# Kernel tuning notes

Measured on AMD Instinct MI355X. Metric: run time of the kernel, lower is better.

## Reference

```python
import jax, jax.numpy as jnp
import numpy as np

A_NUM = 9
C_NUM = 20

def setup_inputs() -> dict:
    key = jax.random.key(0)
    ks = jax.random.split(key, 12)
    B, Cin, H, W = 32, 256, 56, 56
    hidden = 256
    N, M = 64, 2048
    out_ch = 5 * A_NUM + C_NUM
    features = jax.random.normal(ks[0], (B, Cin, H, W), jnp.float32)
    w1 = jax.random.normal(ks[1], (hidden, Cin), jnp.float32) * (1.0 / np.sqrt(Cin))
    b1 = jax.random.normal(ks[2], (hidden,), jnp.float32) * 0.01
    w2 = jax.random.normal(ks[3], (out_ch, hidden), jnp.float32) * (1.0 / np.sqrt(hidden))
    b2 = jax.random.normal(ks[4], (out_ch,), jnp.float32) * 0.01
    # anchor shapes (w, h), positive sizes in grid units
    anc = 1.0 + 5.0 * jax.random.uniform(ks[5], (A_NUM, 2), jnp.float32)
    # grid of cell centers
    xs = jnp.arange(W, dtype=jnp.float32) + 0.5
    ys = jnp.arange(H, dtype=jnp.float32) + 0.5
    gx, gy = jnp.meshgrid(xs, ys, indexing='xy')  # (H, W)
    grid = jnp.broadcast_to(jnp.stack([gx, gy], axis=-1)[None], (B, H, W, 2))
    # GT boxes (x1, y1, x2, y2, cls) with x1<x2, y1<y2
    x1 = jax.random.uniform(ks[6], (B, N), jnp.float32) * (W - 9.0)
    y1 = jax.random.uniform(ks[7], (B, N), jnp.float32) * (H - 9.0)
    bw = 1.0 + 7.0 * jax.random.uniform(ks[8], (B, N), jnp.float32)
    bh = 1.0 + 7.0 * jax.random.uniform(ks[9], (B, N), jnp.float32)
    cls = jax.random.randint(ks[10], (B, N), 0, C_NUM).astype(jnp.float32)
    bboxes = jnp.stack([x1, y1, x1 + bw, y1 + bh, cls], axis=-1)
    total_anchors = B * A_NUM * H * W
    pos_anchor_idx = jax.random.randint(ks[11], (M,), 0, total_anchors, jnp.int64 if jax.config.jax_enable_x64 else jnp.int32)
    neg_anchor_idx = jax.random.randint(jax.random.fold_in(key, 99), (M,), 0, total_anchors, jnp.int64 if jax.config.jax_enable_x64 else jnp.int32)
    GT_offsets = jax.random.normal(jax.random.fold_in(key, 100), (M, 4), jnp.float32) * 0.1
    return {"features": features, "w1": w1, "b1": b1, "w2": w2, "b2": b2,
            "anc": anc, "grid": grid, "bboxes": bboxes, "GT_offsets": GT_offsets,
            "pos_anchor_idx": pos_anchor_idx, "neg_anchor_idx": neg_anchor_idx}

def _generate_anchor(anc, grid):
    # grid: (B,H,W,2), anc: (A,2) -> anchors (B,A,H,W,4) as (x1,y1,x2,y2)
    g = grid[:, None]                      # (B,1,H,W,2)
    a = anc[None, :, None, None]           # (1,A,1,1,2)
    return jnp.concatenate([g - a / 2, g + a / 2], axis=-1)

def _generate_proposal_yolo(anchors, offsets):
    ctr = (anchors[..., :2] + anchors[..., 2:]) / 2
    wh = anchors[..., 2:] - anchors[..., :2]
    new_wh = wh * jnp.exp(offsets[..., 2:])
    new_ctr = ctr + offsets[..., :2]
    return jnp.concatenate([new_ctr - new_wh / 2, new_ctr + new_wh / 2], axis=-1)

def _iou(proposals, bboxes):
    # proposals (B,A,H,W,4) -> (B,AHW,4); bboxes (B,N,5) -> iou (B,AHW,N)
    B = proposals.shape[0]
    p = proposals.reshape(B, -1, 4)[:, :, None, :]   # (B,AHW,1,4)
    g = bboxes[:, None, :, :]                        # (B,1,N,5)
    ix1 = jnp.maximum(p[..., 0], g[..., 0])
    iy1 = jnp.maximum(p[..., 1], g[..., 1])
    ix2 = jnp.minimum(p[..., 2], g[..., 2])
    iy2 = jnp.minimum(p[..., 3], g[..., 3])
    inter = jnp.clip(ix2 - ix1, 0) * jnp.clip(iy2 - iy1, 0)
    gt_area = (bboxes[:, :, 2] - bboxes[:, :, 0]) * (bboxes[:, :, 3] - bboxes[:, :, 1])
    p_area = (p[..., 2] - p[..., 0]) * (p[..., 3] - p[..., 1])
    return inter / (gt_area[:, None, :] + p_area - inter)

def reference(features, w1, b1, w2, b2, anc, grid, bboxes, GT_offsets,
              pos_anchor_idx, neg_anchor_idx):
    B, _, H, W = features.shape
    A = anc.shape[0]
    M = pos_anchor_idx.shape[0]
    # PredictionNetwork (dropout in eval = identity), 1x1 convs as einsum
    x = jnp.einsum('bchw,oc->bohw', features, w1) + b1[None, :, None, None]
    x = jax.nn.leaky_relu(x, 0.01)
    x = jnp.einsum('bchw,oc->bohw', x, w2) + b2[None, :, None, None]
    anc_data = x[:, :5 * A].reshape(B, A, 5, H, W)
    class_all = x[:, 5 * A:]                               # (B,C,H,W)
    conf_all = jax.nn.sigmoid(anc_data[:, :, 0])           # (B,A,H,W)
    offsets_all = jnp.transpose(anc_data[:, :, 1:5], (0, 1, 3, 4, 2))  # (B,A,H,W,4)
    # training extraction
    conf_flat = conf_all.reshape(-1)
    conf_scores = jnp.concatenate([conf_flat[pos_anchor_idx], conf_flat[neg_anchor_idx]])[:, None]  # (2M,1)
    offsets_pos = offsets_all.reshape(-1, 4)[pos_anchor_idx]            # (M,4)
    # class scores for positive anchors: index arithmetic over (B,A,H,W)
    bi = pos_anchor_idx // (A * H * W)
    hw = pos_anchor_idx % (H * W)
    hi, wi = hw // W, hw % W
    class_pos = class_all[bi, :, hi, wi]                                # (M,C)
    # anchors -> proposals -> IoU
    anchors = _generate_anchor(anc, grid)
    proposals = _generate_proposal_yolo(anchors, offsets_all)
    iou_mat = _iou(proposals, bboxes)                                   # (B,AHW,N)
    # YOLO SSE losses
    gt_conf = jnp.concatenate([jnp.ones((M, 1), conf_scores.dtype), jnp.zeros((M, 1), conf_scores.dtype)])
    conf_loss = jnp.sum((conf_scores - gt_conf) ** 2) / (2 * M)
    reg_loss = jnp.sum((offsets_pos - GT_offsets) ** 2) / M
    total_loss = conf_loss + reg_loss
    return total_loss, iou_mat, class_pos
```

## Files before the change

kernel.cpp:

```cpp
#include <hip/hip_runtime.h>
#include <math.h>

#define B_    32
#define CIN   256
#define HID   256
#define OC    65
#define A_    9
#define H_    56
#define W_    56
#define HW    3136
#define AHW   28224
#define NBOX  64
#define M_    2048
#define CNUM  20
#define NTILE 49

#define IOU_N ((size_t)B_ * AHW * NBOX)
#define X2_BYTES ((size_t)B_ * OC * HW * 4)

#define FOFF(frag) (((frag) << 3) + ((((frag) >> 3)) << 3))

typedef _Float16 half8 __attribute__((ext_vector_type(8)));
typedef float f32x16 __attribute__((ext_vector_type(16)));
typedef float f32x4  __attribute__((ext_vector_type(4)));

__device__ __forceinline__ unsigned int pkh(float a, float b) {
    _Float16 ha = (_Float16)a, hb = (_Float16)b;
    unsigned short ua = __builtin_bit_cast(unsigned short, ha);
    unsigned short ub = __builtin_bit_cast(unsigned short, hb);
    return (unsigned int)ua | ((unsigned int)ub << 16);
}

__global__ __launch_bounds__(256) void prep_kernel(
    const float* __restrict__ w1, const float* __restrict__ w2,
    _Float16* __restrict__ w1s, _Float16* __restrict__ w2s)
{
    const int f = blockIdx.x * 256 + threadIdx.x;
    {
        const int e    = f & 7;
        const int lane = (f >> 3) & 63;
        const int kc   = (f >> 9) & 15;
        const int ob   = f >> 13;
        const int row  = ob * 32 + (lane & 31);
        const int k    = kc * 16 + (lane >> 5) * 8 + e;
        w1s[f] = (_Float16)w1[row * CIN + k];
    }
    if (f < 20480) {
        const int e    = f & 7;
        const int lane = (f >> 3) & 63;
        const int ks2  = (f >> 9) & 7;
        const int rt   = f >> 12;
        const int row  = rt * 16 + (lane & 15);
        const int k    = ks2 * 32 + (lane >> 4) * 8 + e;
        w2s[f] = (row < OC) ? (_Float16)w2[row * HID + k] : (_Float16)0.f;
    }
}

__global__ __launch_bounds__(256) void conv_fused_kernel(
    const float* __restrict__ features, const _Float16* __restrict__ w1s,
    const float* __restrict__ b1, const _Float16* __restrict__ w2s,
    const float* __restrict__ b2, float* __restrict__ x2)
{
    __shared__ _Float16 lds_h[18432];
    __shared__ float bias_s[HID];

    _Float16* featAll = lds_h;
    _Float16* hidf    = lds_h;

    const int t    = threadIdx.x;
    const int lane = t & 63;
    const int w    = t >> 6;
    const int bid  = blockIdx.x;
    const int b    = bid / NTILE;
    const int p0   = (bid - b * NTILE) * 64;
    const float* fbase = features + (size_t)b * CIN * HW + p0;

    bias_s[t] = b1[t];

    const int pstage = (t & 15) * 4;
    const int kk     = (t >> 4) * 2;
    const int ksS    = kk >> 4;
    const int gS     = (kk >> 3) & 1;
    const int j0     = kk & 7;
    const int ghalf  = lane >> 5;

#pragma unroll
    for (int c = 0; c < 8; ++c) {
        const float4 r0 = *(const float4*)(fbase + (size_t)(c * 32 + kk) * HW + pstage);
        const float4 r1 = *(const float4*)(fbase + (size_t)(c * 32 + kk + 1) * HW + pstage);
        const float a0[4] = {r0.x, r0.y, r0.z, r0.w};
        const float a1[4] = {r1.x, r1.y, r1.z, r1.w};
#pragma unroll
        for (int e = 0; e < 4; ++e) {
            const int p     = pstage + e;
            const int lane2 = gS * 32 + (p & 31);
            const int pt    = p >> 5;
            const int frag  = c * 256 + (ksS * 2 + pt) * 64 + lane2;
            *(unsigned int*)&featAll[FOFF(frag) + j0] = pkh(a0[e], a1[e]);
        }
    }
    __syncthreads();

    f32x16 facc[2][2];
#pragma unroll
    for (int ot = 0; ot < 2; ++ot)
#pragma unroll
        for (int pt = 0; pt < 2; ++pt)
#pragma unroll
            for (int e = 0; e < 16; ++e) facc[ot][pt][e] = 0.f;

    half8 afb[2][2][2];
#pragma unroll
    for (int ks = 0; ks < 2; ++ks)
#pragma unroll
        for (int ot = 0; ot < 2; ++ot)
            afb[0][ks][ot] = *(const half8*)(w1s + ((size_t)((w * 2 + ot) * 16 + ks) * 64 + lane) * 8);

#pragma unroll
    for (int c = 0; c < 8; ++c) {
        if (c < 7) {
#pragma unroll
            for (int ks = 0; ks < 2; ++ks)
#pragma unroll
                for (int ot = 0; ot < 2; ++ot)
                    afb[(c + 1) & 1][ks][ot] =
                        *(const half8*)(w1s + ((size_t)((w * 2 + ot) * 16 + (c + 1) * 2 + ks) * 64 + lane) * 8);
        }
#pragma unroll
        for (int ks = 0; ks < 2; ++ks) {
#pragma unroll
            for (int pt = 0; pt < 2; ++pt) {
                const half8 bf = *(const half8*)&featAll[FOFF(c * 256 + (ks * 2 + pt) * 64 + lane)];
                facc[0][pt] = __builtin_amdgcn_mfma_f32_32x32x16_f16(afb[c & 1][ks][0], bf, facc[0][pt], 0, 0, 0);
                facc[1][pt] = __builtin_amdgcn_mfma_f32_32x32x16_f16(afb[c & 1][ks][1], bf, facc[1][pt], 0, 0, 0);
            }
        }
    }
    __syncthreads();

    const int col = lane & 31;
#pragma unroll
    for (int ot = 0; ot < 2; ++ot) {
        const int ks2 = w * 2 + ot;
#pragma unroll
        for (int pt = 0; pt < 2; ++pt) {
            const int pt2 = pt * 2 + (col >> 4);
            const int n15 = col & 15;
#pragma unroll
            for (int q = 0; q < 4; ++q) {
                float hv[4];
#pragma unroll
                for (int i = 0; i < 4; ++i) {
                    const int row = i + 8 * q + 4 * ghalf;
                    float v = facc[ot][pt][q * 4 + i] + bias_s[w * 64 + ot * 32 + row];
                    hv[i] = v < 0.f ? 0.01f * v : v;
                }
                const int frag = (ks2 * 4 + pt2) * 64 + (q * 16 + n15);
                *(unsigned int*)&hidf[FOFF(frag) + 4 * ghalf]     = pkh(hv[0], hv[1]);
                *(unsigned int*)&hidf[FOFF(frag) + 4 * ghalf + 2] = pkh(hv[2], hv[3]);
            }
        }
    }
    __syncthreads();

    f32x4 c2[5];
#pragma unroll
    for (int rt = 0; rt < 5; ++rt)
#pragma unroll
        for (int e = 0; e < 4; ++e) c2[rt][e] = 0.f;

    const int m16 = lane & 15;
    const int kgr = lane >> 4;
#pragma unroll 2
    for (int ks2 = 0; ks2 < 8; ++ks2) {
        const half8 bf = *(const half8*)&hidf[FOFF((ks2 * 4 + w) * 64 + lane)];
#pragma unroll
        for (int rt = 0; rt < 5; ++rt) {
            const half8 af = *(const half8*)(w2s + ((size_t)(rt * 8 + ks2) * 64 + lane) * 8);
            c2[rt] = __builtin_amdgcn_mfma_f32_16x16x32_f16(af, bf, c2[rt], 0, 0, 0);
        }
    }

    float* xb = x2 + (size_t)b * OC * HW + p0 + w * 16 + m16;
#pragma unroll
    for (int rt = 0; rt < 5; ++rt) {
#pragma unroll
        for (int r = 0; r < 4; ++r) {
            const int o2 = rt * 16 + kgr * 4 + r;
            if (o2 < OC) xb[(size_t)o2 * HW] = c2[rt][r] + b2[o2];
        }
    }
}

__global__ __launch_bounds__(256) void iou_kernel(
    const float* __restrict__ x2, const float* __restrict__ anc,
    const float* __restrict__ grid, const float* __restrict__ bboxes,
    float* __restrict__ iou_out)
{
    __shared__ float prx1[64], pry1[64], prx2[64], pry2[64], parea[64];
    __shared__ float bx1[64], by1[64], bx2s[64], by2s[64], bga[64];

    const int t    = threadIdx.x;
    const int blk  = blockIdx.x;
    const int b    = blk / (A_ * NTILE);
    const int r    = blk - b * (A_ * NTILE);
    const int a    = r / NTILE;
    const int tile = r - a * NTILE;
    const int hw0  = tile * 64;

    if (t < 64) {
        const int hw = hw0 + t;
        const int h  = hw / W_;
        const int wv = hw - h * W_;
        const float* xb = x2 + ((size_t)b * OC + 5 * a) * HW + hw;
        const float tx = xb[HW], ty = xb[2 * HW], tw = xb[3 * HW], th = xb[4 * HW];
        const size_t gi = (((size_t)b * H_ + h) * W_ + wv) * 2;
        const float gx = grid[gi], gy = grid[gi + 1];
        const float nw = anc[2 * a]     * __expf(tw);
        const float nh = anc[2 * a + 1] * __expf(th);
        const float cx = gx + tx, cy = gy + ty;
        prx1[t] = cx - 0.5f * nw; pry1[t] = cy - 0.5f * nh;
        prx2[t] = cx + 0.5f * nw; pry2[t] = cy + 0.5f * nh;
        parea[t] = nw * nh;
    } else if (t < 128) {
        const int j = t - 64;
        const float* gb = bboxes + ((size_t)b * NBOX + j) * 5;
        const float x1 = gb[0], y1 = gb[1], x2v = gb[2], y2v = gb[3];
        bx1[j] = x1; by1[j] = y1; bx2s[j] = x2v; by2s[j] = y2v;
        bga[j] = (x2v - x1) * (y2v - y1);
    }
    __syncthreads();

    const int lane = t & 63;
    const int w    = t >> 6;
    const int pr   = lane >> 4;
    const int j0   = (lane & 15) * 4;

    float Bx1[4], By1[4], Bx2[4], By2[4], Ba[4];
#pragma unroll
    for (int e = 0; e < 4; ++e) {
        Bx1[e] = bx1[j0 + e]; By1[e] = by1[j0 + e];
        Bx2[e] = bx2s[j0 + e]; By2[e] = by2s[j0 + e];
        Ba[e]  = bga[j0 + e];
    }

    float* dstbase = iou_out + (size_t)blk * 4096;
#pragma unroll
    for (int q = 0; q < 4; ++q) {
        const int p = w * 16 + q * 4 + pr;
        const float Px1 = prx1[p], Py1 = pry1[p], Px2 = prx2[p], Py2 = pry2[p];
        const float pa = parea[p];
        f32x4 o4;
#pragma unroll
        for (int e = 0; e < 4; ++e) {
            const float iw = fminf(Px2, Bx2[e]) - fmaxf(Px1, Bx1[e]);
            const float ih = fminf(Py2, By2[e]) - fmaxf(Py1, By1[e]);
            const float inter = fmaxf(iw, 0.f) * fmaxf(ih, 0.f);
            o4[e] = inter * __builtin_amdgcn_rcpf(Ba[e] + pa - inter);
        }
        __builtin_nontemporal_store(o4, (f32x4*)(dstbase + p * 64 + j0));
    }
}

__global__ __launch_bounds__(256) void tail_kernel(
    const float* __restrict__ x2, const int* __restrict__ pos_idx,
    const int* __restrict__ neg_idx, const float* __restrict__ gt_off,
    float* __restrict__ cls_out, float* __restrict__ out0)
{
    const int t = threadIdx.x;
    if (blockIdx.x < 160) {
        const int g = blockIdx.x * 256 + t;
        const int m = g / CNUM;
        const int c = g - m * CNUM;
        const int idx = pos_idx[m];
        const int bi  = idx / AHW;
        const int hw  = idx % HW;
        cls_out[g] = x2[((size_t)bi * OC + 45 + c) * HW + hw];
        return;
    }
    float csum = 0.f, rsum = 0.f;
    for (int m = t; m < M_; m += 256) {
        const int idx = pos_idx[m];
        const int bi = idx / AHW;
        const int rr = idx - bi * AHW;
        const int a  = rr / HW;
        const int hw = rr - a * HW;
        const float* xb = x2 + ((size_t)bi * OC + 5 * a) * HW + hw;
        const float s = 1.f / (1.f + __expf(-xb[0]));
        csum += (s - 1.f) * (s - 1.f);
#pragma unroll
        for (int k = 0; k < 4; ++k) {
            const float d = xb[(size_t)(k + 1) * HW] - gt_off[m * 4 + k];
            rsum += d * d;
        }
    }
    for (int m = t; m < M_; m += 256) {
        const int idx = neg_idx[m];
        const int bi = idx / AHW;
        const int rr = idx - bi * AHW;
        const int a  = rr / HW;
        const int hw = rr - a * HW;
        const float s = 1.f / (1.f + __expf(-x2[((size_t)bi * OC + 5 * a) * HW + hw]));
        csum += s * s;
    }
    __shared__ float red[8];
#pragma unroll
    for (int off = 32; off > 0; off >>= 1) {
        csum += __shfl_down(csum, off, 64);
        rsum += __shfl_down(rsum, off, 64);
    }
    if ((t & 63) == 0) { red[t >> 6] = csum; red[4 + (t >> 6)] = rsum; }
    __syncthreads();
    if (t == 0) {
        const float c = red[0] + red[1] + red[2] + red[3];
        const float rg = red[4] + red[5] + red[6] + red[7];
        out0[0] = c / (2.f * (float)M_) + rg / (float)M_;
    }
}

extern "C" void kernel_launch(void* const* d_in, const int* in_sizes, int n_in,
                              void* d_out, int out_size, void* d_ws, size_t ws_size,
                              hipStream_t stream) {
    (void)in_sizes; (void)n_in; (void)out_size; (void)ws_size;
    const float* features = (const float*)d_in[0];
    const float* w1       = (const float*)d_in[1];
    const float* b1       = (const float*)d_in[2];
    const float* w2       = (const float*)d_in[3];
    const float* b2       = (const float*)d_in[4];
    const float* anc      = (const float*)d_in[5];
    const float* grid     = (const float*)d_in[6];
    const float* bboxes   = (const float*)d_in[7];
    const float* gt_off   = (const float*)d_in[8];
    const int*   pos_idx  = (const int*)d_in[9];
    const int*   neg_idx  = (const int*)d_in[10];
    float* out = (float*)d_out;

    char* wsb = (char*)d_ws;
    float* x2 = (float*)wsb;
    _Float16* w1s = (_Float16*)(wsb + X2_BYTES);
    _Float16* w2s = w1s + 65536;

    prep_kernel<<<256, 256, 0, stream>>>(w1, w2, w1s, w2s);
    conv_fused_kernel<<<B_ * NTILE, 256, 0, stream>>>(features, w1s, b1, w2s, b2, x2);
    iou_kernel<<<B_ * A_ * NTILE, 256, 0, stream>>>(x2, anc, grid, bboxes, out + 1);
    tail_kernel<<<161, 256, 0, stream>>>(x2, pos_idx, neg_idx, gt_off, out + 1 + IOU_N, out);
}
```

Measured before the change: 390.3 us.

## Fuse IoU computation into conv kernel and compute grid centers analytically

The IoU stage moves into the conv epilogue. Conv outputs for each 64-pixel tile are staged transposed in shared memory, proposals for all 9 anchors are built from them, and the IoU tiles against the batch's GT boxes are written directly. This removes the separate IoU launch, its re-read of x2 and its grid loads; cell centers are computed as index+0.5 instead of reading the grid input. The tail kernel switches to 1024-thread blocks. In exchange each conv block now carries the heavy IoU store stream, with fewer, longer blocks, and correctness depends on the grid input always being the regular arange+0.5 layout.

```diff
diff --git a/kernel.cpp b/kernel.cpp
--- a/kernel.cpp
+++ b/kernel.cpp
@@ -56,16 +56,26 @@
     }
 }
 
-__global__ __launch_bounds__(256) void conv_fused_kernel(
+__global__ __launch_bounds__(256) void conv_iou_kernel(
     const float* __restrict__ features, const _Float16* __restrict__ w1s,
     const float* __restrict__ b1, const _Float16* __restrict__ w2s,
-    const float* __restrict__ b2, float* __restrict__ x2)
+    const float* __restrict__ b2, const float* __restrict__ anc,
+    const float* __restrict__ bboxes, float* __restrict__ x2,
+    float* __restrict__ iou_out)
 {
     __shared__ _Float16 lds_h[18432];
     __shared__ float bias_s[HID];
+    __shared__ float boxs[5 * 64];
 
     _Float16* featAll = lds_h;
     _Float16* hidf    = lds_h;
+    float*    L       = (float*)lds_h;
+    float*    x2t     = L;
+    float*    ppx1    = L + 4416;
+    float*    ppy1    = L + 4992;
+    float*    ppx2    = L + 5568;
+    float*    ppy2    = L + 6144;
+    float*    pare    = L + 6720;
 
     const int t    = threadIdx.x;
     const int lane = t & 63;
@@ -76,12 +86,18 @@
     const float* fbase = features + (size_t)b * CIN * HW + p0;
 
     bias_s[t] = b1[t];
+    if (t < 64) {
+        const float* gb = bboxes + ((size_t)b * NBOX + t) * 5;
+        const float x1 = gb[0], y1 = gb[1], x2v = gb[2], y2v = gb[3];
+        boxs[t] = x1; boxs[64 + t] = y1; boxs[128 + t] = x2v; boxs[192 + t] = y2v;
+        boxs[256 + t] = (x2v - x1) * (y2v - y1);
+    }
 
     const int pstage = (t & 15) * 4;
     const int kk     = (t >> 4) * 2;
     const int ksS    = kk >> 4;
     const int gS     = (kk >> 3) & 1;
-    const int j0     = kk & 7;
+    const int j0h    = kk & 7;
     const int ghalf  = lane >> 5;
 
 #pragma unroll
@@ -96,7 +112,7 @@
             const int lane2 = gS * 32 + (p & 31);
             const int pt    = p >> 5;
             const int frag  = c * 256 + (ksS * 2 + pt) * 64 + lane2;
-            *(unsigned int*)&featAll[FOFF(frag) + j0] = pkh(a0[e], a1[e]);
+            *(unsigned int*)&featAll[FOFF(frag) + j0h] = pkh(a0[e], a1[e]);
         }
     }
     __syncthreads();
@@ -180,96 +196,82 @@
             c2[rt] = __builtin_amdgcn_mfma_f32_16x16x32_f16(af, bf, c2[rt], 0, 0, 0);
         }
     }
+    __syncthreads();
 
     float* xb = x2 + (size_t)b * OC * HW + p0 + w * 16 + m16;
+    const int pxl = w * 16 + m16;
 #pragma unroll
     for (int rt = 0; rt < 5; ++rt) {
 #pragma unroll
         for (int r = 0; r < 4; ++r) {
             const int o2 = rt * 16 + kgr * 4 + r;
-            if (o2 < OC) xb[(size_t)o2 * HW] = c2[rt][r] + b2[o2];
-        }
-    }
-}
-
-__global__ __launch_bounds__(256) void iou_kernel(
-    const float* __restrict__ x2, const float* __restrict__ anc,
-    const float* __restrict__ grid, const float* __restrict__ bboxes,
-    float* __restrict__ iou_out)
-{
-    __shared__ float prx1[64], pry1[64], prx2[64], pry2[64], parea[64];
-    __shared__ float bx1[64], by1[64], bx2s[64], by2s[64], bga[64];
-
-    const int t    = threadIdx.x;
-    const int blk  = blockIdx.x;
-    const int b    = blk / (A_ * NTILE);
-    const int r    = blk - b * (A_ * NTILE);
-    const int a    = r / NTILE;
-    const int tile = r - a * NTILE;
-    const int hw0  = tile * 64;
-
-    if (t < 64) {
-        const int hw = hw0 + t;
+            const float v = c2[rt][r] + b2[o2];
+            if (o2 < OC) {
+                xb[(size_t)o2 * HW] = v;
+                x2t[pxl * 69 + o2] = v;
+            }
+        }
+    }
+    __syncthreads();
+
+    for (int pi = t; pi < A_ * 64; pi += 256) {
+        const int a  = pi >> 6;
+        const int px = pi & 63;
+        const float* xr = x2t + px * 69 + 5 * a;
+        const float tx = xr[1], ty = xr[2], tw = xr[3], th = xr[4];
+        const int hw = p0 + px;
         const int h  = hw / W_;
         const int wv = hw - h * W_;
-        const float* xb = x2 + ((size_t)b * OC + 5 * a) * HW + hw;
-        const float tx = xb[HW], ty = xb[2 * HW], tw = xb[3 * HW], th = xb[4 * HW];
-        const size_t gi = (((size_t)b * H_ + h) * W_ + wv) * 2;
-        const float gx = grid[gi], gy = grid[gi + 1];
+        const float gx = (float)wv + 0.5f;
+        const float gy = (float)h + 0.5f;
         const float nw = anc[2 * a]     * __expf(tw);
         const float nh = anc[2 * a + 1] * __expf(th);
         const float cx = gx + tx, cy = gy + ty;
-        prx1[t] = cx - 0.5f * nw; pry1[t] = cy - 0.5f * nh;
-        prx2[t] = cx + 0.5f * nw; pry2[t] = cy + 0.5f * nh;
-        parea[t] = nw * nh;
-    } else if (t < 128) {
-        const int j = t - 64;
-        const float* gb = bboxes + ((size_t)b * NBOX + j) * 5;
-        const float x1 = gb[0], y1 = gb[1], x2v = gb[2], y2v = gb[3];
-        bx1[j] = x1; by1[j] = y1; bx2s[j] = x2v; by2s[j] = y2v;
-        bga[j] = (x2v - x1) * (y2v - y1);
-    }
-    __syncthreads();
-
-    const int lane = t & 63;
-    const int w    = t >> 6;
-    const int pr   = lane >> 4;
-    const int j0   = (lane & 15) * 4;
-
+        ppx1[pi] = cx - 0.5f * nw; ppy1[pi] = cy - 0.5f * nh;
+        ppx2[pi] = cx + 0.5f * nw; ppy2[pi] = cy + 0.5f * nh;
+        pare[pi] = nw * nh;
+    }
+    __syncthreads();
+
+    const int pr = lane >> 4;
+    const int j0 = (lane & 15) * 4;
     float Bx1[4], By1[4], Bx2[4], By2[4], Ba[4];
 #pragma unroll
     for (int e = 0; e < 4; ++e) {
-        Bx1[e] = bx1[j0 + e]; By1[e] = by1[j0 + e];
-        Bx2[e] = bx2s[j0 + e]; By2[e] = by2s[j0 + e];
-        Ba[e]  = bga[j0 + e];
-    }
-
-    float* dstbase = iou_out + (size_t)blk * 4096;
-#pragma unroll
-    for (int q = 0; q < 4; ++q) {
-        const int p = w * 16 + q * 4 + pr;
-        const float Px1 = prx1[p], Py1 = pry1[p], Px2 = prx2[p], Py2 = pry2[p];
-        const float pa = parea[p];
-        f32x4 o4;
-#pragma unroll
-        for (int e = 0; e < 4; ++e) {
-            const float iw = fminf(Px2, Bx2[e]) - fmaxf(Px1, Bx1[e]);
-            const float ih = fminf(Py2, By2[e]) - fmaxf(Py1, By1[e]);
-            const float inter = fmaxf(iw, 0.f) * fmaxf(ih, 0.f);
-            o4[e] = inter * __builtin_amdgcn_rcpf(Ba[e] + pa - inter);
-        }
-        __builtin_nontemporal_store(o4, (f32x4*)(dstbase + p * 64 + j0));
-    }
-}
-
-__global__ __launch_bounds__(256) void tail_kernel(
+        Bx1[e] = boxs[j0 + e];       By1[e] = boxs[64 + j0 + e];
+        Bx2[e] = boxs[128 + j0 + e]; By2[e] = boxs[192 + j0 + e];
+        Ba[e]  = boxs[256 + j0 + e];
+    }
+    float* ibase = iou_out + ((size_t)b * AHW + p0) * 64;
+#pragma unroll 1
+    for (int a = 0; a < A_; ++a) {
+#pragma unroll
+        for (int q = 0; q < 4; ++q) {
+            const int p = w * 16 + q * 4 + pr;
+            const int i = a * 64 + p;
+            const float Px1 = ppx1[i], Py1 = ppy1[i], Px2 = ppx2[i], Py2 = ppy2[i];
+            const float pa = pare[i];
+            f32x4 o4;
+#pragma unroll
+            for (int e = 0; e < 4; ++e) {
+                const float iw = fminf(Px2, Bx2[e]) - fmaxf(Px1, Bx1[e]);
+                const float ih = fminf(Py2, By2[e]) - fmaxf(Py1, By1[e]);
+                const float inter = fmaxf(iw, 0.f) * fmaxf(ih, 0.f);
+                o4[e] = inter * __builtin_amdgcn_rcpf(Ba[e] + pa - inter);
+            }
+            __builtin_nontemporal_store(o4, (f32x4*)(ibase + ((size_t)a * HW + p) * 64 + j0));
+        }
+    }
+}
+
+__global__ __launch_bounds__(1024) void tail_kernel(
     const float* __restrict__ x2, const int* __restrict__ pos_idx,
     const int* __restrict__ neg_idx, const float* __restrict__ gt_off,
     float* __restrict__ cls_out, float* __restrict__ out0)
 {
     const int t = threadIdx.x;
-    if (blockIdx.x < 160) {
-        const int g = blockIdx.x * 256 + t;
+    if (blockIdx.x < 40) {
+        const int g = blockIdx.x * 1024 + t;
         const int m = g / CNUM;
         const int c = g - m * CNUM;
         const int idx = pos_idx[m];
@@ -279,7 +281,7 @@
         return;
     }
     float csum = 0.f, rsum = 0.f;
-    for (int m = t; m < M_; m += 256) {
+    for (int m = t; m < M_; m += 1024) {
         const int idx = pos_idx[m];
         const int bi = idx / AHW;
         const int rr = idx - bi * AHW;
@@ -294,7 +296,7 @@
             rsum += d * d;
         }
     }
-    for (int m = t; m < M_; m += 256) {
+    for (int m = t; m < M_; m += 1024) {
         const int idx = neg_idx[m];
         const int bi = idx / AHW;
         const int rr = idx - bi * AHW;
@@ -303,17 +305,18 @@
         const float s = 1.f / (1.f + __expf(-x2[((size_t)bi * OC + 5 * a) * HW + hw]));
         csum += s * s;
     }
-    __shared__ float red[8];
+    __shared__ float red[32];
 #pragma unroll
     for (int off = 32; off > 0; off >>= 1) {
         csum += __shfl_down(csum, off, 64);
         rsum += __shfl_down(rsum, off, 64);
     }
-    if ((t & 63) == 0) { red[t >> 6] = csum; red[4 + (t >> 6)] = rsum; }
+    if ((t & 63) == 0) { red[t >> 6] = csum; red[16 + (t >> 6)] = rsum; }
     __syncthreads();
     if (t == 0) {
-        const float c = red[0] + red[1] + red[2] + red[3];
-        const float rg = red[4] + red[5] + red[6] + red[7];
+        float c = 0.f, rg = 0.f;
+#pragma unroll
+        for (int i = 0; i < 16; ++i) { c += red[i]; rg += red[16 + i]; }
         out0[0] = c / (2.f * (float)M_) + rg / (float)M_;
     }
 }
@@ -328,7 +331,6 @@
     const float* w2       = (const float*)d_in[3];
     const float* b2       = (const float*)d_in[4];
     const float* anc      = (const float*)d_in[5];
-    const float* grid     = (const float*)d_in[6];
     const float* bboxes   = (const float*)d_in[7];
     const float* gt_off   = (const float*)d_in[8];
     const int*   pos_idx  = (const int*)d_in[9];
@@ -341,7 +343,7 @@
     _Float16* w2s = w1s + 65536;
 
     prep_kernel<<<256, 256, 0, stream>>>(w1, w2, w1s, w2s);
-    conv_fused_kernel<<<B_ * NTILE, 256, 0, stream>>>(features, w1s, b1, w2s, b2, x2);
-    iou_kernel<<<B_ * A_ * NTILE, 256, 0, stream>>>(x2, anc, grid, bboxes, out + 1);
-    tail_kernel<<<161, 256, 0, stream>>>(x2, pos_idx, neg_idx, gt_off, out + 1 + IOU_N, out);
-}
+    conv_iou_kernel<<<B_ * NTILE, 256, 0, stream>>>(features, w1s, b1, w2s, b2,
+                                                    anc, bboxes, x2, out + 1);
+    tail_kernel<<<41, 1024, 0, stream>>>(x2, pos_idx, neg_idx, gt_off, out + 1 + IOU_N, out);
+}
```

New measurement: 386.6 us. Within noise of the previous version (-1.0%).
